# Performance work log

Hardware: AMD Instinct MI355X
Metric: run time of the kernel (lower is better)

The kernel has to match this reference:

```python
import jax, jax.numpy as jnp
import numpy as np

B, L, N, D = 4096, 50, 50, 128
STD = 0.1


def setup_inputs() -> dict:
    key = jax.random.key(0)
    ks = jax.random.split(key, 6)
    seq_idx = jax.random.randint(ks[0], (B, L), 0, N, dtype=jnp.int32)
    mask = jnp.ones((B, L), dtype=jnp.int32)
    node_vectors = jax.random.normal(ks[1], (B, N, D), dtype=jnp.float32)
    u = lambda k, shp: jax.random.uniform(k, shp, jnp.float32, -STD, STD)
    return {
        "sequence_of_indexes": seq_idx,
        "mask": mask,
        "node_vectors": node_vectors,
        "batch_size": B,
        "W_last": u(ks[2], (D, D)),      # dense_last_item kernel (no bias)
        "W_seq": u(ks[3], (D, D)),       # dense_sequence_items kernel
        "b_seq": jnp.zeros((D,), jnp.float32),  # dense_sequence_items bias
        "W_alpha": u(ks[4], (D, 1)),     # dense_alpha kernel (no bias)
    }


def reference(sequence_of_indexes, mask, node_vectors, batch_size,
              W_last, W_seq, b_seq, W_alpha):
    maskf = mask.astype(jnp.float32)                          # [B, L]
    seq_len = jnp.sum(maskf, axis=1).astype(jnp.int32)        # [B]
    rows = jnp.arange(batch_size)
    # last item index per session, then gather its node vector
    last_idx = sequence_of_indexes[rows, seq_len - 1]         # [B]
    v_n = node_vectors[rows, last_idx]                        # [B, D]
    # per-batch embedding lookup: node_vectors[b, seq_idx[b]]
    v_i = jnp.take_along_axis(node_vectors, sequence_of_indexes[..., None], axis=1)  # [B, L, D]
    vn_proj = (v_n @ W_last)[:, None, :]                      # [B, 1, D]
    vi_proj = v_i @ W_seq + b_seq                             # [B, L, D]
    alpha = jax.nn.sigmoid(vn_proj + vi_proj) @ W_alpha       # [B, L, 1]
    alpha = alpha * maskf[..., None]
    session_graph = jnp.sum(alpha * v_i, axis=1)              # [B, D]
    return v_n, session_graph
```

## Files before the change

### kernel.cpp

```cpp
#include <hip/hip_runtime.h>
#include <hip/hip_bf16.h>
#include <math.h>

#define BB 4096
#define LL 50
#define NN 50
#define DD 128
#define STR 136

typedef short bf16x8 __attribute__((ext_vector_type(8)));
typedef float f32x4  __attribute__((ext_vector_type(4)));

static __device__ inline unsigned short f32_to_bf16_rne(float f) {
    unsigned int u = __float_as_uint(f);
    u += 0x7FFFu + ((u >> 16) & 1u);
    return (unsigned short)(u >> 16);
}
static __device__ inline float bf16_to_f32(unsigned short h) {
    return __uint_as_float(((unsigned int)h) << 16);
}
static __device__ inline unsigned int pack_bf16x2(float x, float y) {
    __hip_bfloat162 h = __float22bfloat162_rn(make_float2(x, y));
    union { __hip_bfloat162 h2; unsigned int u; } c;
    c.h2 = h;
    return c.u;
}

__global__ void prep_w(const float* __restrict__ W_seq,
                       const float* __restrict__ W_last,
                       unsigned short* __restrict__ ws)
{
    int t = blockIdx.x * blockDim.x + threadIdx.x;
    int lane = t & 63;
    int nt   = (t >> 6) & 7;
    int kk   = t >> 9;
    const float* W = (kk < 4) ? W_seq : W_last;
    int kb = (kk & 3) * 32 + (lane >> 4) * 8;
    int n  = nt * 16 + (lane & 15);
    unsigned short* dst = ws + (size_t)t * 8;
    #pragma unroll
    for (int j = 0; j < 8; ++j)
        dst[j] = f32_to_bf16_rne(W[(kb + j) * DD + n]);
}

__global__ __launch_bounds__(256, 3) void sess_attn(
    const int*   __restrict__ seq_idx,
    const int*   __restrict__ mask,
    const float* __restrict__ nodes,
    const float* __restrict__ b_seq,
    const float* __restrict__ W_alpha,
    const unsigned short* __restrict__ wfrag,
    float*       __restrict__ out)
{
    const int b    = blockIdx.x;
    const int tid  = threadIdx.x;
    const int lane = tid & 63;
    const int wave = tid >> 6;
    const int col  = lane & 15;
    const int quad = lane >> 4;

    __shared__ __align__(16) unsigned short s_nbf[64][STR];
    __shared__ float s_alpha[64];
    __shared__ float s_cntf[64];
    __shared__ int   s_last;

    const float4* nb4 = (const float4*)(nodes + (size_t)b * (NN * DD));
    float4 v[6];
    #pragma unroll
    for (int j = 0; j < 6; ++j) v[j] = nb4[tid + j * 256];
    float4 v6;
    if (tid < 64) v6 = nb4[tid + 1536];

    const bf16x8* wsf = (const bf16x8*)wfrag;
    bf16x8 bfS[8];
    #pragma unroll
    for (int kk = 0; kk < 4; ++kk)
        #pragma unroll
        for (int j = 0; j < 2; ++j)
            bfS[kk * 2 + j] = wsf[(size_t)((kk * 8 + wave * 2 + j) * 64 + lane)];

    int pm = 0, pi = 0;
    if (tid < 64) {
        pm = (tid < LL) ? mask[b * LL + tid]    : 0;
        pi = (tid < LL) ? seq_idx[b * LL + tid] : 0;
    }

    float bb_r[2], wa_r[2];
    #pragma unroll
    for (int j = 0; j < 2; ++j) {
        int n = (wave * 2 + j) * 16 + col;
        bb_r[j] = b_seq[n];
        wa_r[j] = W_alpha[n];
    }

    if (tid < 64) { s_alpha[tid] = 0.f; s_cntf[tid] = 0.f; }

    #pragma unroll
    for (int j = 0; j < 6; ++j) {
        int idx = tid + j * 256;
        int r = idx >> 5, c = (idx & 31) * 4;
        uint2 hh;
        hh.x = pack_bf16x2(v[j].x, v[j].y);
        hh.y = pack_bf16x2(v[j].z, v[j].w);
        *(uint2*)&s_nbf[r][c] = hh;
    }
    if (tid < 64) {
        int idx = tid + 1536;
        int r = idx >> 5, c = (idx & 31) * 4;
        uint2 hh;
        hh.x = pack_bf16x2(v6.x, v6.y);
        hh.y = pack_bf16x2(v6.z, v6.w);
        *(uint2*)&s_nbf[r][c] = hh;
    }

    if (tid < 64) {
        int mm = pm;
        mm += __shfl_xor(mm, 1);  mm += __shfl_xor(mm, 2);
        mm += __shfl_xor(mm, 4);  mm += __shfl_xor(mm, 8);
        mm += __shfl_xor(mm, 16); mm += __shfl_xor(mm, 32);
        int j = mm - 1;
        if (j < 0) j += LL;
        int li = __shfl(pi, j);
        if (tid == 0) s_last = li;
        if (tid < LL && pm) atomicAdd(&s_cntf[pi], (float)pm);
    }
    __syncthreads();

    const int last = s_last;

    bf16x8 bfL[8];
    #pragma unroll
    for (int kk = 0; kk < 4; ++kk)
        #pragma unroll
        for (int j = 0; j < 2; ++j)
            bfL[kk * 2 + j] = wsf[(size_t)(((kk + 4) * 8 + wave * 2 + j) * 64 + lane)];

    f32x4 acc[4][2];
    #pragma unroll
    for (int m = 0; m < 4; ++m)
        #pragma unroll
        for (int j = 0; j < 2; ++j)
            acc[m][j] = (f32x4){0.f, 0.f, 0.f, 0.f};

    #pragma unroll
    for (int kk = 0; kk < 4; ++kk) {
        bf16x8 a[4];
        #pragma unroll
        for (int m = 0; m < 4; ++m)
            a[m] = *(const bf16x8*)&s_nbf[m * 16 + col][kk * 32 + quad * 8];
        #pragma unroll
        for (int j = 0; j < 2; ++j)
            #pragma unroll
            for (int m = 0; m < 4; ++m)
                acc[m][j] = __builtin_amdgcn_mfma_f32_16x16x32_bf16(
                    a[m], bfS[kk * 2 + j], acc[m][j], 0, 0, 0);
    }

    f32x4 accV[2];
    #pragma unroll
    for (int j = 0; j < 2; ++j)
        accV[j] = (f32x4){bb_r[j], bb_r[j], bb_r[j], bb_r[j]};
    #pragma unroll
    for (int kk = 0; kk < 4; ++kk) {
        bf16x8 av = *(const bf16x8*)&s_nbf[last][kk * 32 + quad * 8];
        #pragma unroll
        for (int j = 0; j < 2; ++j)
            accV[j] = __builtin_amdgcn_mfma_f32_16x16x32_bf16(
                av, bfL[kk * 2 + j], accV[j], 0, 0, 0);
    }

    #pragma unroll
    for (int m = 0; m < 4; ++m) {
        float pr[4] = {0.f, 0.f, 0.f, 0.f};
        #pragma unroll
        for (int j = 0; j < 2; ++j) {
            float wa = wa_r[j];
            #pragma unroll
            for (int r = 0; r < 4; ++r) {
                float x = acc[m][j][r] + accV[j][r];
                float sig = __builtin_amdgcn_rcpf(1.f + __expf(-x));
                pr[r] = fmaf(sig, wa, pr[r]);
            }
        }
        #pragma unroll
        for (int r = 0; r < 4; ++r) {
            float vv = pr[r];
            vv += __shfl_xor(vv, 1);
            vv += __shfl_xor(vv, 2);
            vv += __shfl_xor(vv, 4);
            vv += __shfl_xor(vv, 8);
            int row = m * 16 + quad * 4 + r;
            if (col == 0 && row < NN) atomicAdd(&s_alpha[row], vv);
        }
    }
    __syncthreads();

    if (tid < DD) {
        float acc2 = 0.f;
        #pragma unroll 10
        for (int n = 0; n < NN; ++n)
            acc2 = fmaf(s_cntf[n] * s_alpha[n], bf16_to_f32(s_nbf[n][tid]), acc2);
        out[(size_t)BB * DD + (size_t)b * DD + tid] = acc2;
        out[(size_t)b * DD + tid] = bf16_to_f32(s_nbf[last][tid]);
    }
}

extern "C" void kernel_launch(void* const* d_in, const int* in_sizes, int n_in,
                              void* d_out, int out_size, void* d_ws, size_t ws_size,
                              hipStream_t stream) {
    const int*   seq     = (const int*)  d_in[0];
    const int*   mask    = (const int*)  d_in[1];
    const float* nodes   = (const float*)d_in[2];
    const float* W_last  = (const float*)d_in[4];
    const float* W_seq   = (const float*)d_in[5];
    const float* b_seq   = (const float*)d_in[6];
    const float* W_alpha = (const float*)d_in[7];
    float*       out     = (float*)      d_out;

    unsigned short* wsf = (unsigned short*)d_ws;

    prep_w<<<16, 256, 0, stream>>>(W_seq, W_last, wsf);
    sess_attn<<<BB, 256, 0, stream>>>(seq, mask, nodes, b_seq, W_alpha, wsf, out);
}
```

Measured before the change: 188.1 us.

## Stage fp32 node vectors into LDS via async global_load_lds, convert on read

```diff
diff --git a/kernel.cpp b/kernel.cpp
--- a/kernel.cpp
+++ b/kernel.cpp
@@ -6,7 +6,6 @@
 #define LL 50
 #define NN 50
 #define DD 128
-#define STR 136
 
 typedef short bf16x8 __attribute__((ext_vector_type(8)));
 typedef float f32x4  __attribute__((ext_vector_type(4)));
@@ -15,15 +14,27 @@
     unsigned int u = __float_as_uint(f);
     u += 0x7FFFu + ((u >> 16) & 1u);
     return (unsigned short)(u >> 16);
-}
-static __device__ inline float bf16_to_f32(unsigned short h) {
-    return __uint_as_float(((unsigned int)h) << 16);
 }
 static __device__ inline unsigned int pack_bf16x2(float x, float y) {
     __hip_bfloat162 h = __float22bfloat162_rn(make_float2(x, y));
     union { __hip_bfloat162 h2; unsigned int u; } c;
     c.h2 = h;
     return c.u;
+}
+static __device__ inline bf16x8 frag_from_f32(const float* p) {
+    float4 lo = *(const float4*)p;
+    float4 hi = *(const float4*)(p + 4);
+    union { unsigned int u[4]; bf16x8 v; } c;
+    c.u[0] = pack_bf16x2(lo.x, lo.y);
+    c.u[1] = pack_bf16x2(lo.z, lo.w);
+    c.u[2] = pack_bf16x2(hi.x, hi.y);
+    c.u[3] = pack_bf16x2(hi.z, hi.w);
+    return c.v;
+}
+static __device__ inline void async_copy16(const void* g, void* l) {
+    __builtin_amdgcn_global_load_lds(
+        (const __attribute__((address_space(1))) void*)g,
+        (__attribute__((address_space(3))) void*)l, 16, 0, 0);
 }
 
 __global__ void prep_w(const float* __restrict__ W_seq,
@@ -43,7 +54,7 @@
         dst[j] = f32_to_bf16_rne(W[(kb + j) * DD + n]);
 }
 
-__global__ __launch_bounds__(256, 3) void sess_attn(
+__global__ __launch_bounds__(256, 4) void sess_attn(
     const int*   __restrict__ seq_idx,
     const int*   __restrict__ mask,
     const float* __restrict__ nodes,
@@ -59,25 +70,25 @@
     const int col  = lane & 15;
     const int quad = lane >> 4;
 
-    __shared__ __align__(16) unsigned short s_nbf[64][STR];
+    __shared__ __align__(16) float s_nf[NN * DD];
     __shared__ float s_alpha[64];
     __shared__ float s_cntf[64];
     __shared__ int   s_last;
 
-    const float4* nb4 = (const float4*)(nodes + (size_t)b * (NN * DD));
-    float4 v[6];
-    #pragma unroll
-    for (int j = 0; j < 6; ++j) v[j] = nb4[tid + j * 256];
-    float4 v6;
-    if (tid < 64) v6 = nb4[tid + 1536];
+    const char* gsrc = (const char*)(nodes + (size_t)b * (NN * DD));
+    char* lbase = (char*)s_nf;
+    for (int c = wave; c < 25; c += 4)
+        async_copy16(gsrc + c * 1024 + lane * 16, lbase + c * 1024);
 
     const bf16x8* wsf = (const bf16x8*)wfrag;
-    bf16x8 bfS[8];
+    bf16x8 bfS[8], bfL[8];
     #pragma unroll
     for (int kk = 0; kk < 4; ++kk)
         #pragma unroll
-        for (int j = 0; j < 2; ++j)
-            bfS[kk * 2 + j] = wsf[(size_t)((kk * 8 + wave * 2 + j) * 64 + lane)];
+        for (int j = 0; j < 2; ++j) {
+            bfS[kk * 2 + j] = wsf[(size_t)(((kk    ) * 8 + wave * 2 + j) * 64 + lane)];
+            bfL[kk * 2 + j] = wsf[(size_t)(((kk + 4) * 8 + wave * 2 + j) * 64 + lane)];
+        }
 
     int pm = 0, pi = 0;
     if (tid < 64) {
@@ -94,24 +105,6 @@
     }
 
     if (tid < 64) { s_alpha[tid] = 0.f; s_cntf[tid] = 0.f; }
-
-    #pragma unroll
-    for (int j = 0; j < 6; ++j) {
-        int idx = tid + j * 256;
-        int r = idx >> 5, c = (idx & 31) * 4;
-        uint2 hh;
-        hh.x = pack_bf16x2(v[j].x, v[j].y);
-        hh.y = pack_bf16x2(v[j].z, v[j].w);
-        *(uint2*)&s_nbf[r][c] = hh;
-    }
-    if (tid < 64) {
-        int idx = tid + 1536;
-        int r = idx >> 5, c = (idx & 31) * 4;
-        uint2 hh;
-        hh.x = pack_bf16x2(v6.x, v6.y);
-        hh.y = pack_bf16x2(v6.z, v6.w);
-        *(uint2*)&s_nbf[r][c] = hh;
-    }
 
     if (tid < 64) {
         int mm = pm;
@@ -128,12 +121,18 @@
 
     const int last = s_last;
 
-    bf16x8 bfL[8];
-    #pragma unroll
-    for (int kk = 0; kk < 4; ++kk)
+    f32x4 accV[2];
+    #pragma unroll
+    for (int j = 0; j < 2; ++j)
+        accV[j] = (f32x4){bb_r[j], bb_r[j], bb_r[j], bb_r[j]};
+    #pragma unroll
+    for (int kk = 0; kk < 4; ++kk) {
+        bf16x8 av = frag_from_f32(&s_nf[last * DD + kk * 32 + quad * 8]);
         #pragma unroll
         for (int j = 0; j < 2; ++j)
-            bfL[kk * 2 + j] = wsf[(size_t)(((kk + 4) * 8 + wave * 2 + j) * 64 + lane)];
+            accV[j] = __builtin_amdgcn_mfma_f32_16x16x32_bf16(
+                av, bfL[kk * 2 + j], accV[j], 0, 0, 0);
+    }
 
     f32x4 acc[4][2];
     #pragma unroll
@@ -146,27 +145,16 @@
     for (int kk = 0; kk < 4; ++kk) {
         bf16x8 a[4];
         #pragma unroll
-        for (int m = 0; m < 4; ++m)
-            a[m] = *(const bf16x8*)&s_nbf[m * 16 + col][kk * 32 + quad * 8];
+        for (int m = 0; m < 4; ++m) {
+            int row = m * 16 + col;
+            a[m] = frag_from_f32(&s_nf[row * DD + kk * 32 + quad * 8]);
+        }
         #pragma unroll
         for (int j = 0; j < 2; ++j)
             #pragma unroll
             for (int m = 0; m < 4; ++m)
                 acc[m][j] = __builtin_amdgcn_mfma_f32_16x16x32_bf16(
                     a[m], bfS[kk * 2 + j], acc[m][j], 0, 0, 0);
-    }
-
-    f32x4 accV[2];
-    #pragma unroll
-    for (int j = 0; j < 2; ++j)
-        accV[j] = (f32x4){bb_r[j], bb_r[j], bb_r[j], bb_r[j]};
-    #pragma unroll
-    for (int kk = 0; kk < 4; ++kk) {
-        bf16x8 av = *(const bf16x8*)&s_nbf[last][kk * 32 + quad * 8];
-        #pragma unroll
-        for (int j = 0; j < 2; ++j)
-            accV[j] = __builtin_amdgcn_mfma_f32_16x16x32_bf16(
-                av, bfL[kk * 2 + j], accV[j], 0, 0, 0);
     }
 
     #pragma unroll
@@ -199,9 +187,9 @@
         float acc2 = 0.f;
         #pragma unroll 10
         for (int n = 0; n < NN; ++n)
-            acc2 = fmaf(s_cntf[n] * s_alpha[n], bf16_to_f32(s_nbf[n][tid]), acc2);
+            acc2 = fmaf(s_cntf[n] * s_alpha[n], s_nf[n * DD + tid], acc2);
         out[(size_t)BB * DD + (size_t)b * DD + tid] = acc2;
-        out[(size_t)b * DD + tid] = bf16_to_f32(s_nbf[last][tid]);
+        out[(size_t)b * DD + tid] = s_nf[last * DD + tid];
     }
 }
 
```

Result: slower. 192.6 us (+2.4%).
